# Performance work log

Measured on AMD Instinct MI355X. Metric: run time of the kernel, lower is better.

Reference implementation:

```python
import jax, jax.numpy as jnp
import numpy as np

HIDDEN = 512

def setup_inputs() -> dict:
    key = jax.random.key(0)
    ks = jax.random.split(key, 6)
    B, T = 65536, 100
    scale = 0.1  # keep tanh MLP in a sane dynamic range
    return {
        "y0": jax.random.normal(ks[0], (B, 2), jnp.float32),
        "t_points": jnp.arange(T, dtype=jnp.float32) * 0.01,
        "W1": jax.random.normal(ks[1], (2, HIDDEN), jnp.float32) * scale,
        "b1": jnp.zeros((HIDDEN,), jnp.float32),
        "W2": jax.random.normal(ks[2], (HIDDEN, HIDDEN), jnp.float32) * scale,
        "b2": jnp.zeros((HIDDEN,), jnp.float32),
        "W3": jax.random.normal(ks[3], (HIDDEN, HIDDEN // 2), jnp.float32) * scale,
        "b3": jnp.zeros((HIDDEN // 2,), jnp.float32),
        "W4": jax.random.normal(ks[4], (HIDDEN // 2, 2), jnp.float32) * scale,
        "b4": jnp.zeros((2,), jnp.float32),
    }

def _mlp(y, W1, b1, W2, b2, W3, b3, W4, b4):
    # 4-layer tanh MLP: 2 -> H -> H -> H//2 -> 2 (t is unused in ODEFunc)
    h = jnp.tanh(y @ W1 + b1)
    h = jnp.tanh(h @ W2 + b2)
    h = jnp.tanh(h @ W3 + b3)
    return h @ W4 + b4

def reference(y0, t_points, W1, b1, W2, b2, W3, b3, W4, b4):
    f = lambda y: _mlp(y, W1, b1, W2, b2, W3, b3, W4, b4)
    dts = t_points[1:] - t_points[:-1]  # [T-1]

    def step(y, dt):
        k1 = f(y)
        k2 = f(y + k1 * (dt * 0.5))
        k3 = f(y + k2 * (dt * 0.5))
        k4 = f(y + k3 * dt)
        y_next = y + (dt / 6.0) * (k1 + 2.0 * k2 + 2.0 * k3 + k4)
        return y_next, y_next

    _, traj = jax.lax.scan(step, y0, dts)
    return jnp.concatenate([y0[None], traj], axis=0)  # [T, B, 2]
```

## Files before the change

kernel.cpp:

```cpp
#include <hip/hip_runtime.h>
#include <hip/hip_bf16.h>
#include <stdint.h>

using bfrag_t = __attribute__((ext_vector_type(8))) short;
using f32x4   = __attribute__((ext_vector_type(4))) float;

#define HID  512
#define H3   256
#define RB   128
#define NTH  512
#define KSC  2.885390081777927f

static __device__ __forceinline__ uint32_t bf16_rne(float f) {
    uint32_t u = __float_as_uint(f);
    return (u + 0x7fffu + ((u >> 16) & 1u)) >> 16;
}
static __device__ __forceinline__ uint32_t pk_bf16(float a, float b) {
    union { __hip_bfloat162 h; uint32_t u; } c;
    c.h = __float22bfloat162_rn(make_float2(a, b));
    return c.u;
}
static __device__ __forceinline__ float fast_exp2(float x) {
#if __has_builtin(__builtin_amdgcn_exp2f)
    return __builtin_amdgcn_exp2f(x);
#else
    return exp2f(x);
#endif
}
static __device__ __forceinline__ float fast_rcp(float x) {
#if __has_builtin(__builtin_amdgcn_rcpf)
    return __builtin_amdgcn_rcpf(x);
#else
    return 1.0f / x;
#endif
}
static __device__ __forceinline__ float ftanh_s(float xs) {
    float e = fast_exp2(xs);
    return 1.0f - 2.0f * fast_rcp(e + 1.0f);
}
static __device__ __forceinline__ bfrag_t frag_of(uint4 v) {
    union { uint4 u; bfrag_t f; } c; c.u = v; return c.f;
}

__global__ void prep_weights(const float* __restrict__ W1, const float* __restrict__ b1,
                             const float* __restrict__ W2, const float* __restrict__ b2,
                             const float* __restrict__ W3, const float* __restrict__ b3,
                             uint4* __restrict__ o2, uint4* __restrict__ o3,
                             float* __restrict__ w1p, float* __restrict__ b2s,
                             float* __restrict__ b3s)
{
    int id = blockIdx.x * 256 + threadIdx.x;
    if (id < 32768) {
        int l = id & 63, kt = (id >> 6) & 15, mt = id >> 10;
        int m = mt * 16 + (l & 15), k0 = kt * 32 + (l >> 4) * 8;
        uint32_t p[4];
        #pragma unroll
        for (int jj = 0; jj < 4; ++jj) {
            float v0 = KSC * W2[(k0 + jj * 2    ) * 512 + m];
            float v1 = KSC * W2[(k0 + jj * 2 + 1) * 512 + m];
            p[jj] = bf16_rne(v0) | (bf16_rne(v1) << 16);
        }
        o2[id] = make_uint4(p[0], p[1], p[2], p[3]);
    } else if (id < 49152) {
        int id2 = id - 32768;
        int l = id2 & 63, kt = (id2 >> 6) & 15, mt = id2 >> 10;
        int m = mt * 16 + (l & 15), k0 = kt * 32 + (l >> 4) * 8;
        uint32_t p[4];
        #pragma unroll
        for (int jj = 0; jj < 4; ++jj) {
            float v0 = KSC * W3[(k0 + jj * 2    ) * 256 + m];
            float v1 = KSC * W3[(k0 + jj * 2 + 1) * 256 + m];
            p[jj] = bf16_rne(v0) | (bf16_rne(v1) << 16);
        }
        o3[id2] = make_uint4(p[0], p[1], p[2], p[3]);
    } else if (id < 49152 + 1536) {
        int t = id - 49152;
        int ck = t / 24, j = t % 24;
        int f = ck * 8 + (j & 7);
        float v = (j < 8) ? W1[f] : (j < 16) ? W1[512 + f] : b1[f];
        w1p[t] = KSC * v;
    } else if (id < 49152 + 1536 + 512) {
        int i = id - 49152 - 1536; b2s[i] = KSC * b2[i];
    } else if (id < 49152 + 1536 + 512 + 256) {
        int i = id - 49152 - 1536 - 512; b3s[i] = KSC * b3[i];
    }
}

struct SmemT {
    uint4  hbuf[64 * RB];
    float  b2[HID];
    float  b3[H3];
    float  y [RB][2];
    float  z [RB][2];
    float  ya[RB][2];
    float  part[4][RB][2];
};

__global__ __launch_bounds__(NTH, 2) void node_kernel(
    const float* __restrict__ y0, const float* __restrict__ tp,
    const float* __restrict__ W4g, const float* __restrict__ b4g,
    const uint4* __restrict__ w2A, const uint4* __restrict__ w3A,
    const float* __restrict__ w1p, const float* __restrict__ b2s,
    const float* __restrict__ b3s,
    float* __restrict__ out, int Bn, int T)
{
    __shared__ SmemT s;
    const int tid = threadIdx.x;
    const int l   = tid & 63;
    const int w   = tid >> 6;
    const int wu  = __builtin_amdgcn_readfirstlane(w);
    const int b0  = blockIdx.x * RB;

    for (int i = tid; i < HID; i += NTH) s.b2[i] = b2s[i];
    for (int i = tid; i < H3;  i += NTH) s.b3[i] = b3s[i];
    if (tid < RB) {
        float2 v = ((const float2*)y0)[b0 + tid];
        s.y[tid][0] = v.x; s.y[tid][1] = v.y;
        ((float2*)out)[b0 + tid] = v;
    }
    __syncthreads();

    const float* w1w = w1p + wu * 8 * 24;

    for (int st = 0; st < T - 1; ++st) {
        float dt = tp[st + 1] - tp[st];
        if (tid < RB) {
            s.z [tid][0] = s.y[tid][0]; s.z [tid][1] = s.y[tid][1];
            s.ya[tid][0] = s.y[tid][0]; s.ya[tid][1] = s.y[tid][1];
        }
        __syncthreads();

        for (int e = 0; e < 4; ++e) {
            {
                float zl0 = s.z[l][0],      zl1 = s.z[l][1];
                float zh0 = s.z[64 + l][0], zh1 = s.z[64 + l][1];
                #pragma unroll
                for (int i = 0; i < 8; ++i) {
                    const float* P = w1w + i * 24;
                    int ck = wu * 8 + i;
                    float xa[8], xb[8];
                    #pragma unroll
                    for (int jj = 0; jj < 8; ++jj) {
                        float wa = P[jj], wb = P[8 + jj], bb = P[16 + jj];
                        xa[jj] = ftanh_s(fmaf(zl0, wa, fmaf(zl1, wb, bb)));
                        xb[jj] = ftanh_s(fmaf(zh0, wa, fmaf(zh1, wb, bb)));
                    }
                    s.hbuf[ck * RB + l] = make_uint4(
                        pk_bf16(xa[0], xa[1]), pk_bf16(xa[2], xa[3]),
                        pk_bf16(xa[4], xa[5]), pk_bf16(xa[6], xa[7]));
                    s.hbuf[ck * RB + 64 + l] = make_uint4(
                        pk_bf16(xb[0], xb[1]), pk_bf16(xb[2], xb[3]),
                        pk_bf16(xb[4], xb[5]), pk_bf16(xb[6], xb[7]));
                }
            }
            __syncthreads();

            {
                const int q = l >> 4, rr = l & 15;
                f32x4 acc[4][8];
                #pragma unroll
                for (int mt = 0; mt < 4; ++mt) {
                    int mb = (w * 4 + mt) * 16 + q * 4;
                    float4 bi = *(const float4*)&s.b2[mb];
                    #pragma unroll
                    for (int nt = 0; nt < 8; ++nt) acc[mt][nt] = (f32x4){bi.x, bi.y, bi.z, bi.w};
                }
                uint4 aC[4], aN[4];
                #pragma unroll
                for (int mt = 0; mt < 4; ++mt) aC[mt] = w2A[((w * 4 + mt) * 16) * 64 + l];
                for (int kt = 0; kt < 16; ++kt) {
                    uint4 bF[8];
                    #pragma unroll
                    for (int nt = 0; nt < 8; ++nt)
                        bF[nt] = s.hbuf[(kt * 4 + q) * RB + nt * 16 + rr];
                    if (kt < 15) {
                        #pragma unroll
                        for (int mt = 0; mt < 4; ++mt)
                            aN[mt] = w2A[(((w * 4 + mt) * 16) + kt + 1) * 64 + l];
                    }
                    #pragma unroll
                    for (int mt = 0; mt < 4; ++mt)
                        #pragma unroll
                        for (int nt = 0; nt < 8; ++nt)
                            acc[mt][nt] = __builtin_amdgcn_mfma_f32_16x16x32_bf16(
                                frag_of(aC[mt]), frag_of(bF[nt]), acc[mt][nt], 0, 0, 0);
                    #pragma unroll
                    for (int mt = 0; mt < 4; ++mt) aC[mt] = aN[mt];
                }
                __syncthreads();
                #pragma unroll
                for (int mt = 0; mt < 4; ++mt) {
                    int mb = (w * 4 + mt) * 16 + q * 4;
                    int ck = mb >> 3, hi = (mb >> 2) & 1;
                    #pragma unroll
                    for (int nt = 0; nt < 8; ++nt) {
                        int n = nt * 16 + rr;
                        f32x4 c = acc[mt][nt];
                        uint32_t u0 = pk_bf16(ftanh_s(c[0]), ftanh_s(c[1]));
                        uint32_t u1 = pk_bf16(ftanh_s(c[2]), ftanh_s(c[3]));
                        ((uint2*)s.hbuf)[((ck * RB + n) << 1) | hi] = make_uint2(u0, u1);
                    }
                }
                __syncthreads();
            }

            {
                const int q = l >> 4, rr = l & 15;
                const int mg = w >> 1, ng = w & 1;
                f32x4 acc[4][4];
                #pragma unroll
                for (int mt = 0; mt < 4; ++mt) {
                    int mb = (mg * 4 + mt) * 16 + q * 4;
                    float4 bi = *(const float4*)&s.b3[mb];
                    #pragma unroll
                    for (int nt = 0; nt < 4; ++nt) acc[mt][nt] = (f32x4){bi.x, bi.y, bi.z, bi.w};
                }
                uint4 aC[4], aN[4];
                #pragma unroll
                for (int mt = 0; mt < 4; ++mt) aC[mt] = w3A[((mg * 4 + mt) * 16) * 64 + l];
                for (int kt = 0; kt < 16; ++kt) {
                    uint4 bF[4];
                    #pragma unroll
                    for (int nt = 0; nt < 4; ++nt)
                        bF[nt] = s.hbuf[(kt * 4 + q) * RB + ng * 64 + nt * 16 + rr];
                    if (kt < 15) {
                        #pragma unroll
                        for (int mt = 0; mt < 4; ++mt)
                            aN[mt] = w3A[(((mg * 4 + mt) * 16) + kt + 1) * 64 + l];
                    }
                    #pragma unroll
                    for (int mt = 0; mt < 4; ++mt)
                        #pragma unroll
                        for (int nt = 0; nt < 4; ++nt)
                            acc[mt][nt] = __builtin_amdgcn_mfma_f32_16x16x32_bf16(
                                frag_of(aC[mt]), frag_of(bF[nt]), acc[mt][nt], 0, 0, 0);
                    #pragma unroll
                    for (int mt = 0; mt < 4; ++mt) aC[mt] = aN[mt];
                }
                __syncthreads();
                #pragma unroll
                for (int mt = 0; mt < 4; ++mt) {
                    int mb = (mg * 4 + mt) * 16 + q * 4;
                    int ck = mb >> 3, hi = (mb >> 2) & 1;
                    #pragma unroll
                    for (int nt = 0; nt < 4; ++nt) {
                        int n = ng * 64 + nt * 16 + rr;
                        f32x4 c = acc[mt][nt];
                        uint32_t u0 = pk_bf16(ftanh_s(c[0]), ftanh_s(c[1]));
                        uint32_t u1 = pk_bf16(ftanh_s(c[2]), ftanh_s(c[3]));
                        ((uint2*)s.hbuf)[((ck * RB + n) << 1) | hi] = make_uint2(u0, u1);
                    }
                }
                __syncthreads();
            }

            {
                int r  = tid & 127;
                int qq = __builtin_amdgcn_readfirstlane(tid >> 7);
                float a0 = 0.f, a1 = 0.f;
                #pragma unroll
                for (int j = 0; j < 8; ++j) {
                    int ck = qq * 8 + j;
                    uint4 hv = s.hbuf[ck * RB + r];
                    const uint32_t* pu = (const uint32_t*)&hv;
                    #pragma unroll
                    for (int jj = 0; jj < 4; ++jj) {
                        uint32_t uu = pu[jj];
                        float h0 = __uint_as_float(uu << 16);
                        float h1 = __uint_as_float(uu & 0xffff0000u);
                        int f = ck * 8 + jj * 2;
                        a0 = fmaf(h0, W4g[f * 2],     fmaf(h1, W4g[f * 2 + 2], a0));
                        a1 = fmaf(h0, W4g[f * 2 + 1], fmaf(h1, W4g[f * 2 + 3], a1));
                    }
                }
                s.part[qq][r][0] = a0; s.part[qq][r][1] = a1;
            }
            __syncthreads();

            if (tid < RB) {
                float k0 = s.part[0][tid][0] + s.part[1][tid][0]
                         + s.part[2][tid][0] + s.part[3][tid][0] + b4g[0];
                float k1 = s.part[0][tid][1] + s.part[1][tid][1]
                         + s.part[2][tid][1] + s.part[3][tid][1] + b4g[1];
                float wg = (e == 0 || e == 3) ? dt * (1.f / 6.f) : dt * (1.f / 3.f);
                s.ya[tid][0] += wg * k0; s.ya[tid][1] += wg * k1;
                if (e < 3) {
                    float aa = (e == 2) ? dt : dt * 0.5f;
                    s.z[tid][0] = s.y[tid][0] + aa * k0;
                    s.z[tid][1] = s.y[tid][1] + aa * k1;
                } else {
                    s.y[tid][0] = s.ya[tid][0]; s.y[tid][1] = s.ya[tid][1];
                    ((float2*)out)[(size_t)(st + 1) * Bn + b0 + tid] =
                        make_float2(s.ya[tid][0], s.ya[tid][1]);
                }
            }
            __syncthreads();
        }
    }
}

extern "C" void kernel_launch(void* const* d_in, const int* in_sizes, int n_in,
                              void* d_out, int out_size, void* d_ws, size_t ws_size,
                              hipStream_t stream)
{
    const float* y0 = (const float*)d_in[0];
    const float* tp = (const float*)d_in[1];
    const float* W1 = (const float*)d_in[2];
    const float* b1 = (const float*)d_in[3];
    const float* W2 = (const float*)d_in[4];
    const float* b2 = (const float*)d_in[5];
    const float* W3 = (const float*)d_in[6];
    const float* b3 = (const float*)d_in[7];
    const float* W4 = (const float*)d_in[8];
    const float* b4 = (const float*)d_in[9];
    float* out = (float*)d_out;

    const int Bn = in_sizes[0] / 2;
    const int T  = in_sizes[1];

    uint4* w2A = (uint4*)d_ws;
    uint4* w3A = w2A + 32768;
    float* w1p = (float*)(w3A + 16384);
    float* b2s = w1p + 1536;
    float* b3s = b2s + 512;

    prep_weights<<<201, 256, 0, stream>>>(W1, b1, W2, b2, W3, b3,
                                          w2A, w3A, w1p, b2s, b3s);
    node_kernel<<<Bn / RB, NTH, 0, stream>>>(y0, tp, W4, b4,
                                             w2A, w3A, w1p, b2s, b3s, out, Bn, T);
}
```

Measured before the change: 26.28 ms.

## Split block rows into two half-batches and interleave MLP stages across them

Each block's 128 rows are split into two 64-row halves with separate hidden buffers, and the RK4 MLP evaluation is software-pipelined so one half's layer-3/layer-4 work overlaps the other half's layer-1/layer-2 work between barriers. The goal is to fill the serial phases (scalar tanh layer 1, the W4 reduction and the RK update), which otherwise leave MFMA units idle, with independent matrix work from the other half. The cost is narrower MFMA tiles per half (fewer B-fragment reuses per weight load, so w2A/w3A are reloaded twice as often), more shared memory, and a more complicated schedule.

```diff
diff --git a/kernel.cpp b/kernel.cpp
--- a/kernel.cpp
+++ b/kernel.cpp
@@ -7,7 +7,7 @@
 
 #define HID  512
 #define H3   256
-#define RB   128
+#define RB   64
 #define NTH  512
 #define KSC  2.885390081777927f
 
@@ -87,14 +87,206 @@
 }
 
 struct SmemT {
-    uint4  hbuf[64 * RB];
+    uint4  hA[64 * RB];
+    uint4  hB[64 * RB];
     float  b2[HID];
     float  b3[H3];
-    float  y [RB][2];
-    float  z [RB][2];
-    float  ya[RB][2];
-    float  part[4][RB][2];
+    float  y [128][2];
+    float  z [128][2];
+    float  ya[128][2];
+    float  part[8][RB][2];
 };
+
+static __device__ __forceinline__ void s1_stage(uint4* __restrict__ h,
+                                                const float* __restrict__ zrow,
+                                                const float* __restrict__ w1w,
+                                                int l, int wu)
+{
+    float z0 = zrow[2 * l], z1 = zrow[2 * l + 1];
+    #pragma unroll
+    for (int i = 0; i < 8; ++i) {
+        const float* P = w1w + i * 24;
+        int ck = wu * 8 + i;
+        float x[8];
+        #pragma unroll
+        for (int jj = 0; jj < 8; ++jj)
+            x[jj] = ftanh_s(fmaf(z0, P[jj], fmaf(z1, P[8 + jj], P[16 + jj])));
+        h[ck * RB + l] = make_uint4(pk_bf16(x[0], x[1]), pk_bf16(x[2], x[3]),
+                                    pk_bf16(x[4], x[5]), pk_bf16(x[6], x[7]));
+    }
+}
+
+static __device__ __forceinline__ void s2_mfma(const uint4* __restrict__ h,
+                                               const uint4* __restrict__ w2A,
+                                               const float* __restrict__ b2,
+                                               f32x4 (&acc)[4][4],
+                                               int l, int w, int q, int rr)
+{
+    #pragma unroll
+    for (int mt = 0; mt < 4; ++mt) {
+        int mb = (w * 4 + mt) * 16 + q * 4;
+        float4 bi = *(const float4*)&b2[mb];
+        #pragma unroll
+        for (int nt = 0; nt < 4; ++nt) acc[mt][nt] = (f32x4){bi.x, bi.y, bi.z, bi.w};
+    }
+    uint4 aC[4], aN[4];
+    #pragma unroll
+    for (int mt = 0; mt < 4; ++mt) aC[mt] = w2A[((w * 4 + mt) * 16) * 64 + l];
+    for (int kt = 0; kt < 16; ++kt) {
+        uint4 bF[4];
+        #pragma unroll
+        for (int nt = 0; nt < 4; ++nt)
+            bF[nt] = h[(kt * 4 + q) * RB + nt * 16 + rr];
+        if (kt < 15) {
+            #pragma unroll
+            for (int mt = 0; mt < 4; ++mt)
+                aN[mt] = w2A[(((w * 4 + mt) * 16) + kt + 1) * 64 + l];
+        }
+        #pragma unroll
+        for (int mt = 0; mt < 4; ++mt)
+            #pragma unroll
+            for (int nt = 0; nt < 4; ++nt)
+                acc[mt][nt] = __builtin_amdgcn_mfma_f32_16x16x32_bf16(
+                    frag_of(aC[mt]), frag_of(bF[nt]), acc[mt][nt], 0, 0, 0);
+        #pragma unroll
+        for (int mt = 0; mt < 4; ++mt) aC[mt] = aN[mt];
+    }
+}
+
+static __device__ __forceinline__ void s2_epi(uint4* __restrict__ h,
+                                              f32x4 (&acc)[4][4],
+                                              int w, int q, int rr)
+{
+    #pragma unroll
+    for (int mt = 0; mt < 4; ++mt) {
+        int mb = (w * 4 + mt) * 16 + q * 4;
+        int ck = mb >> 3, hi = (mb >> 2) & 1;
+        #pragma unroll
+        for (int nt = 0; nt < 4; ++nt) {
+            int n = nt * 16 + rr;
+            f32x4 c = acc[mt][nt];
+            uint32_t u0 = pk_bf16(ftanh_s(c[0]), ftanh_s(c[1]));
+            uint32_t u1 = pk_bf16(ftanh_s(c[2]), ftanh_s(c[3]));
+            ((uint2*)h)[((ck * RB + n) << 1) | hi] = make_uint2(u0, u1);
+        }
+    }
+}
+
+static __device__ __forceinline__ void s3_mfma(const uint4* __restrict__ h,
+                                               const uint4* __restrict__ w3A,
+                                               const float* __restrict__ b3,
+                                               f32x4 (&acc)[2][4],
+                                               int l, int w, int q, int rr)
+{
+    #pragma unroll
+    for (int mt = 0; mt < 2; ++mt) {
+        int mb = (w * 2 + mt) * 16 + q * 4;
+        float4 bi = *(const float4*)&b3[mb];
+        #pragma unroll
+        for (int nt = 0; nt < 4; ++nt) acc[mt][nt] = (f32x4){bi.x, bi.y, bi.z, bi.w};
+    }
+    uint4 aC[2], aN[2];
+    #pragma unroll
+    for (int mt = 0; mt < 2; ++mt) aC[mt] = w3A[((w * 2 + mt) * 16) * 64 + l];
+    for (int kt = 0; kt < 16; ++kt) {
+        uint4 bF[4];
+        #pragma unroll
+        for (int nt = 0; nt < 4; ++nt)
+            bF[nt] = h[(kt * 4 + q) * RB + nt * 16 + rr];
+        if (kt < 15) {
+            #pragma unroll
+            for (int mt = 0; mt < 2; ++mt)
+                aN[mt] = w3A[(((w * 2 + mt) * 16) + kt + 1) * 64 + l];
+        }
+        #pragma unroll
+        for (int mt = 0; mt < 2; ++mt)
+            #pragma unroll
+            for (int nt = 0; nt < 4; ++nt)
+                acc[mt][nt] = __builtin_amdgcn_mfma_f32_16x16x32_bf16(
+                    frag_of(aC[mt]), frag_of(bF[nt]), acc[mt][nt], 0, 0, 0);
+        #pragma unroll
+        for (int mt = 0; mt < 2; ++mt) aC[mt] = aN[mt];
+    }
+}
+
+static __device__ __forceinline__ void s3_epi(uint4* __restrict__ h,
+                                              f32x4 (&acc)[2][4],
+                                              int w, int q, int rr)
+{
+    #pragma unroll
+    for (int mt = 0; mt < 2; ++mt) {
+        int mb = (w * 2 + mt) * 16 + q * 4;
+        int ck = mb >> 3, hi = (mb >> 2) & 1;
+        #pragma unroll
+        for (int nt = 0; nt < 4; ++nt) {
+            int n = nt * 16 + rr;
+            f32x4 c = acc[mt][nt];
+            uint32_t u0 = pk_bf16(ftanh_s(c[0]), ftanh_s(c[1]));
+            uint32_t u1 = pk_bf16(ftanh_s(c[2]), ftanh_s(c[3]));
+            ((uint2*)h)[((ck * RB + n) << 1) | hi] = make_uint2(u0, u1);
+        }
+    }
+}
+
+static __device__ __forceinline__ void s4_part(const uint4* __restrict__ h,
+                                               float* __restrict__ part,
+                                               const float* __restrict__ W4g,
+                                               int tid)
+{
+    int r  = tid & 63;
+    int qq = __builtin_amdgcn_readfirstlane(tid >> 6);
+    float a0 = 0.f, a1 = 0.f;
+    #pragma unroll
+    for (int j = 0; j < 4; ++j) {
+        int ck = qq * 4 + j;
+        uint4 hv = h[ck * RB + r];
+        const uint32_t* pu = (const uint32_t*)&hv;
+        #pragma unroll
+        for (int jj = 0; jj < 4; ++jj) {
+            uint32_t uu = pu[jj];
+            float h0 = __uint_as_float(uu << 16);
+            float h1 = __uint_as_float(uu & 0xffff0000u);
+            int f = ck * 8 + jj * 2;
+            a0 = fmaf(h0, W4g[f * 2],     fmaf(h1, W4g[f * 2 + 2], a0));
+            a1 = fmaf(h0, W4g[f * 2 + 1], fmaf(h1, W4g[f * 2 + 3], a1));
+        }
+    }
+    part[(qq * RB + r) * 2    ] = a0;
+    part[(qq * RB + r) * 2 + 1] = a1;
+}
+
+static __device__ __forceinline__ void s4_fin(float* __restrict__ yS, float* __restrict__ zS,
+                                              float* __restrict__ yaS,
+                                              const float* __restrict__ part,
+                                              const float* __restrict__ tp,
+                                              const float* __restrict__ b4g,
+                                              float* __restrict__ out,
+                                              int g, int Bn, int rowg, int tid)
+{
+    if (tid < RB) {
+        int r = tid;
+        float k0 = b4g[0], k1 = b4g[1];
+        #pragma unroll
+        for (int qq = 0; qq < 8; ++qq) {
+            k0 += part[(qq * RB + r) * 2];
+            k1 += part[(qq * RB + r) * 2 + 1];
+        }
+        int st = g >> 2, e = g & 3;
+        float dt = tp[st + 1] - tp[st];
+        float wg = (e == 0 || e == 3) ? dt * (1.f / 6.f) : dt * (1.f / 3.f);
+        float ya0 = yaS[2 * r] + wg * k0, ya1 = yaS[2 * r + 1] + wg * k1;
+        yaS[2 * r] = ya0; yaS[2 * r + 1] = ya1;
+        if (e < 3) {
+            float aa = (e == 2) ? dt : dt * 0.5f;
+            zS[2 * r] = yS[2 * r] + aa * k0;
+            zS[2 * r + 1] = yS[2 * r + 1] + aa * k1;
+        } else {
+            yS[2 * r] = ya0; yS[2 * r + 1] = ya1;
+            zS[2 * r] = ya0; zS[2 * r + 1] = ya1;
+            ((float2*)out)[(size_t)(st + 1) * Bn + rowg + r] = make_float2(ya0, ya1);
+        }
+    }
+}
 
 __global__ __launch_bounds__(NTH, 2) void node_kernel(
     const float* __restrict__ y0, const float* __restrict__ tp,
@@ -109,191 +301,65 @@
     const int l   = tid & 63;
     const int w   = tid >> 6;
     const int wu  = __builtin_amdgcn_readfirstlane(w);
-    const int b0  = blockIdx.x * RB;
+    const int q   = l >> 4, rr = l & 15;
+    const int b0  = blockIdx.x * 128;
 
     for (int i = tid; i < HID; i += NTH) s.b2[i] = b2s[i];
     for (int i = tid; i < H3;  i += NTH) s.b3[i] = b3s[i];
-    if (tid < RB) {
+    if (tid < 128) {
         float2 v = ((const float2*)y0)[b0 + tid];
         s.y[tid][0] = v.x; s.y[tid][1] = v.y;
+        s.z[tid][0] = v.x; s.z[tid][1] = v.y;
+        s.ya[tid][0] = v.x; s.ya[tid][1] = v.y;
         ((float2*)out)[b0 + tid] = v;
     }
     __syncthreads();
 
-    const float* w1w = w1p + wu * 8 * 24;
-
-    for (int st = 0; st < T - 1; ++st) {
-        float dt = tp[st + 1] - tp[st];
-        if (tid < RB) {
-            s.z [tid][0] = s.y[tid][0]; s.z [tid][1] = s.y[tid][1];
-            s.ya[tid][0] = s.y[tid][0]; s.ya[tid][1] = s.y[tid][1];
-        }
-        __syncthreads();
-
-        for (int e = 0; e < 4; ++e) {
-            {
-                float zl0 = s.z[l][0],      zl1 = s.z[l][1];
-                float zh0 = s.z[64 + l][0], zh1 = s.z[64 + l][1];
-                #pragma unroll
-                for (int i = 0; i < 8; ++i) {
-                    const float* P = w1w + i * 24;
-                    int ck = wu * 8 + i;
-                    float xa[8], xb[8];
-                    #pragma unroll
-                    for (int jj = 0; jj < 8; ++jj) {
-                        float wa = P[jj], wb = P[8 + jj], bb = P[16 + jj];
-                        xa[jj] = ftanh_s(fmaf(zl0, wa, fmaf(zl1, wb, bb)));
-                        xb[jj] = ftanh_s(fmaf(zh0, wa, fmaf(zh1, wb, bb)));
-                    }
-                    s.hbuf[ck * RB + l] = make_uint4(
-                        pk_bf16(xa[0], xa[1]), pk_bf16(xa[2], xa[3]),
-                        pk_bf16(xa[4], xa[5]), pk_bf16(xa[6], xa[7]));
-                    s.hbuf[ck * RB + 64 + l] = make_uint4(
-                        pk_bf16(xb[0], xb[1]), pk_bf16(xb[2], xb[3]),
-                        pk_bf16(xb[4], xb[5]), pk_bf16(xb[6], xb[7]));
-                }
-            }
-            __syncthreads();
-
-            {
-                const int q = l >> 4, rr = l & 15;
-                f32x4 acc[4][8];
-                #pragma unroll
-                for (int mt = 0; mt < 4; ++mt) {
-                    int mb = (w * 4 + mt) * 16 + q * 4;
-                    float4 bi = *(const float4*)&s.b2[mb];
-                    #pragma unroll
-                    for (int nt = 0; nt < 8; ++nt) acc[mt][nt] = (f32x4){bi.x, bi.y, bi.z, bi.w};
-                }
-                uint4 aC[4], aN[4];
-                #pragma unroll
-                for (int mt = 0; mt < 4; ++mt) aC[mt] = w2A[((w * 4 + mt) * 16) * 64 + l];
-                for (int kt = 0; kt < 16; ++kt) {
-                    uint4 bF[8];
-                    #pragma unroll
-                    for (int nt = 0; nt < 8; ++nt)
-                        bF[nt] = s.hbuf[(kt * 4 + q) * RB + nt * 16 + rr];
-                    if (kt < 15) {
-                        #pragma unroll
-                        for (int mt = 0; mt < 4; ++mt)
-                            aN[mt] = w2A[(((w * 4 + mt) * 16) + kt + 1) * 64 + l];
-                    }
-                    #pragma unroll
-                    for (int mt = 0; mt < 4; ++mt)
-                        #pragma unroll
-                        for (int nt = 0; nt < 8; ++nt)
-                            acc[mt][nt] = __builtin_amdgcn_mfma_f32_16x16x32_bf16(
-                                frag_of(aC[mt]), frag_of(bF[nt]), acc[mt][nt], 0, 0, 0);
-                    #pragma unroll
-                    for (int mt = 0; mt < 4; ++mt) aC[mt] = aN[mt];
-                }
-                __syncthreads();
-                #pragma unroll
-                for (int mt = 0; mt < 4; ++mt) {
-                    int mb = (w * 4 + mt) * 16 + q * 4;
-                    int ck = mb >> 3, hi = (mb >> 2) & 1;
-                    #pragma unroll
-                    for (int nt = 0; nt < 8; ++nt) {
-                        int n = nt * 16 + rr;
-                        f32x4 c = acc[mt][nt];
-                        uint32_t u0 = pk_bf16(ftanh_s(c[0]), ftanh_s(c[1]));
-                        uint32_t u1 = pk_bf16(ftanh_s(c[2]), ftanh_s(c[3]));
-                        ((uint2*)s.hbuf)[((ck * RB + n) << 1) | hi] = make_uint2(u0, u1);
-                    }
-                }
-                __syncthreads();
-            }
-
-            {
-                const int q = l >> 4, rr = l & 15;
-                const int mg = w >> 1, ng = w & 1;
-                f32x4 acc[4][4];
-                #pragma unroll
-                for (int mt = 0; mt < 4; ++mt) {
-                    int mb = (mg * 4 + mt) * 16 + q * 4;
-                    float4 bi = *(const float4*)&s.b3[mb];
-                    #pragma unroll
-                    for (int nt = 0; nt < 4; ++nt) acc[mt][nt] = (f32x4){bi.x, bi.y, bi.z, bi.w};
-                }
-                uint4 aC[4], aN[4];
-                #pragma unroll
-                for (int mt = 0; mt < 4; ++mt) aC[mt] = w3A[((mg * 4 + mt) * 16) * 64 + l];
-                for (int kt = 0; kt < 16; ++kt) {
-                    uint4 bF[4];
-                    #pragma unroll
-                    for (int nt = 0; nt < 4; ++nt)
-                        bF[nt] = s.hbuf[(kt * 4 + q) * RB + ng * 64 + nt * 16 + rr];
-                    if (kt < 15) {
-                        #pragma unroll
-                        for (int mt = 0; mt < 4; ++mt)
-                            aN[mt] = w3A[(((mg * 4 + mt) * 16) + kt + 1) * 64 + l];
-                    }
-                    #pragma unroll
-                    for (int mt = 0; mt < 4; ++mt)
-                        #pragma unroll
-                        for (int nt = 0; nt < 4; ++nt)
-                            acc[mt][nt] = __builtin_amdgcn_mfma_f32_16x16x32_bf16(
-                                frag_of(aC[mt]), frag_of(bF[nt]), acc[mt][nt], 0, 0, 0);
-                    #pragma unroll
-                    for (int mt = 0; mt < 4; ++mt) aC[mt] = aN[mt];
-                }
-                __syncthreads();
-                #pragma unroll
-                for (int mt = 0; mt < 4; ++mt) {
-                    int mb = (mg * 4 + mt) * 16 + q * 4;
-                    int ck = mb >> 3, hi = (mb >> 2) & 1;
-                    #pragma unroll
-                    for (int nt = 0; nt < 4; ++nt) {
-                        int n = ng * 64 + nt * 16 + rr;
-                        f32x4 c = acc[mt][nt];
-                        uint32_t u0 = pk_bf16(ftanh_s(c[0]), ftanh_s(c[1]));
-                        uint32_t u1 = pk_bf16(ftanh_s(c[2]), ftanh_s(c[3]));
-                        ((uint2*)s.hbuf)[((ck * RB + n) << 1) | hi] = make_uint2(u0, u1);
-                    }
-                }
-                __syncthreads();
-            }
-
-            {
-                int r  = tid & 127;
-                int qq = __builtin_amdgcn_readfirstlane(tid >> 7);
-                float a0 = 0.f, a1 = 0.f;
-                #pragma unroll
-                for (int j = 0; j < 8; ++j) {
-                    int ck = qq * 8 + j;
-                    uint4 hv = s.hbuf[ck * RB + r];
-                    const uint32_t* pu = (const uint32_t*)&hv;
-                    #pragma unroll
-                    for (int jj = 0; jj < 4; ++jj) {
-                        uint32_t uu = pu[jj];
-                        float h0 = __uint_as_float(uu << 16);
-                        float h1 = __uint_as_float(uu & 0xffff0000u);
-                        int f = ck * 8 + jj * 2;
-                        a0 = fmaf(h0, W4g[f * 2],     fmaf(h1, W4g[f * 2 + 2], a0));
-                        a1 = fmaf(h0, W4g[f * 2 + 1], fmaf(h1, W4g[f * 2 + 3], a1));
-                    }
-                }
-                s.part[qq][r][0] = a0; s.part[qq][r][1] = a1;
-            }
-            __syncthreads();
-
-            if (tid < RB) {
-                float k0 = s.part[0][tid][0] + s.part[1][tid][0]
-                         + s.part[2][tid][0] + s.part[3][tid][0] + b4g[0];
-                float k1 = s.part[0][tid][1] + s.part[1][tid][1]
-                         + s.part[2][tid][1] + s.part[3][tid][1] + b4g[1];
-                float wg = (e == 0 || e == 3) ? dt * (1.f / 6.f) : dt * (1.f / 3.f);
-                s.ya[tid][0] += wg * k0; s.ya[tid][1] += wg * k1;
-                if (e < 3) {
-                    float aa = (e == 2) ? dt : dt * 0.5f;
-                    s.z[tid][0] = s.y[tid][0] + aa * k0;
-                    s.z[tid][1] = s.y[tid][1] + aa * k1;
-                } else {
-                    s.y[tid][0] = s.ya[tid][0]; s.y[tid][1] = s.ya[tid][1];
-                    ((float2*)out)[(size_t)(st + 1) * Bn + b0 + tid] =
-                        make_float2(s.ya[tid][0], s.ya[tid][1]);
-                }
-            }
+    const float* w1w = w1p + wu * 192;
+    float* part = &s.part[0][0][0];
+    const int E = (T - 1) * 4;
+
+    for (int ea = 0; ea <= E; ++ea) {
+        const bool doA = (ea < E), doB = (ea > 0);
+        const int gB = ea - 1;
+
+        {
+            f32x4 c3[2][4];
+            if (doB) s3_mfma(s.hB, w3A, s.b3, c3, l, w, q, rr);
+            if (doA) s1_stage(s.hA, &s.z[0][0], w1w, l, wu);
+            __syncthreads();
+            if (doB) s3_epi(s.hB, c3, w, q, rr);
+            __syncthreads();
+        }
+
+        {
+            f32x4 c2[4][4];
+            if (doA) s2_mfma(s.hA, w2A, s.b2, c2, l, w, q, rr);
+            if (doB) s4_part(s.hB, part, W4g, tid);
+            __syncthreads();
+            if (doA) s2_epi(s.hA, c2, w, q, rr);
+            if (doB) s4_fin(&s.y[64][0], &s.z[64][0], &s.ya[64][0], part,
+                            tp, b4g, out, gB, Bn, b0 + 64, tid);
+            __syncthreads();
+        }
+
+        {
+            f32x4 c3[2][4];
+            if (doA) s3_mfma(s.hA, w3A, s.b3, c3, l, w, q, rr);
+            if (doA) s1_stage(s.hB, &s.z[64][0], w1w, l, wu);
+            __syncthreads();
+            if (doA) s3_epi(s.hA, c3, w, q, rr);
+            __syncthreads();
+        }
+
+        {
+            f32x4 c2[4][4];
+            if (doA) s2_mfma(s.hB, w2A, s.b2, c2, l, w, q, rr);
+            if (doA) s4_part(s.hA, part, W4g, tid);
+            __syncthreads();
+            if (doA) s2_epi(s.hB, c2, w, q, rr);
+            if (doA) s4_fin(&s.y[0][0], &s.z[0][0], &s.ya[0][0], part,
+                            tp, b4g, out, ea, Bn, b0, tid);
             __syncthreads();
         }
     }
@@ -326,6 +392,6 @@
 
     prep_weights<<<201, 256, 0, stream>>>(W1, b1, W2, b2, W3, b3,
                                           w2A, w3A, w1p, b2s, b3s);
-    node_kernel<<<Bn / RB, NTH, 0, stream>>>(y0, tp, W4, b4,
-                                             w2A, w3A, w1p, b2s, b3s, out, Bn, T);
-}
+    node_kernel<<<Bn / 128, NTH, 0, stream>>>(y0, tp, W4, b4,
+                                              w2A, w3A, w1p, b2s, b3s, out, Bn, T);
+}
```

Measured after the change: 67.70 ms. 158% more time.

## Halve rows per block and switch layer GEMMs to 32x32x16 MFMA tiles

Applied to the files above, without the earlier changes.

Block row count drops from 128 to 64, and the hidden-layer GEMMs now use 32x32x16 bf16 MFMA with 16-wide accumulators instead of 16x16x32 tiles. The weight pre-pack layout is rewritten to match, and launch bounds now ask for 4 blocks per CU. The intent is more resident blocks per CU to hide latency and fewer, larger MFMA ops. In exchange, each weight fragment read from global memory is reused across half as many rows, so weight traffic per row doubles. The W4 reduction is split over 8 waves and reads its weights as float4.

```diff
diff --git a/kernel.cpp b/kernel.cpp
--- a/kernel.cpp
+++ b/kernel.cpp
@@ -3,11 +3,11 @@
 #include <stdint.h>
 
 using bfrag_t = __attribute__((ext_vector_type(8))) short;
-using f32x4   = __attribute__((ext_vector_type(4))) float;
+using f32x16  = __attribute__((ext_vector_type(16))) float;
 
 #define HID  512
 #define H3   256
-#define RB   128
+#define RB   64
 #define NTH  512
 #define KSC  2.885390081777927f
 
@@ -51,8 +51,8 @@
 {
     int id = blockIdx.x * 256 + threadIdx.x;
     if (id < 32768) {
-        int l = id & 63, kt = (id >> 6) & 15, mt = id >> 10;
-        int m = mt * 16 + (l & 15), k0 = kt * 32 + (l >> 4) * 8;
+        int l = id & 63, kt = (id >> 6) & 31, mt = id >> 11;
+        int m = mt * 32 + (l & 31), k0 = kt * 16 + (l >> 5) * 8;
         uint32_t p[4];
         #pragma unroll
         for (int jj = 0; jj < 4; ++jj) {
@@ -63,8 +63,8 @@
         o2[id] = make_uint4(p[0], p[1], p[2], p[3]);
     } else if (id < 49152) {
         int id2 = id - 32768;
-        int l = id2 & 63, kt = (id2 >> 6) & 15, mt = id2 >> 10;
-        int m = mt * 16 + (l & 15), k0 = kt * 32 + (l >> 4) * 8;
+        int l = id2 & 63, kt = (id2 >> 6) & 31, mt = id2 >> 11;
+        int m = mt * 32 + (l & 31), k0 = kt * 16 + (l >> 5) * 8;
         uint32_t p[4];
         #pragma unroll
         for (int jj = 0; jj < 4; ++jj) {
@@ -93,10 +93,10 @@
     float  y [RB][2];
     float  z [RB][2];
     float  ya[RB][2];
-    float  part[4][RB][2];
+    float  part[8][RB][2];
 };
 
-__global__ __launch_bounds__(NTH, 2) void node_kernel(
+__global__ __launch_bounds__(NTH, 4) void node_kernel(
     const float* __restrict__ y0, const float* __restrict__ tp,
     const float* __restrict__ W4g, const float* __restrict__ b4g,
     const uint4* __restrict__ w2A, const uint4* __restrict__ w3A,
@@ -109,6 +109,7 @@
     const int l   = tid & 63;
     const int w   = tid >> 6;
     const int wu  = __builtin_amdgcn_readfirstlane(w);
+    const int q2  = l >> 5, r32 = l & 31;
     const int b0  = blockIdx.x * RB;
 
     for (int i = tid; i < HID; i += NTH) s.b2[i] = b2s[i];
@@ -120,7 +121,7 @@
     }
     __syncthreads();
 
-    const float* w1w = w1p + wu * 8 * 24;
+    const float* w1w = w1p + wu * 192;
 
     for (int st = 0; st < T - 1; ++st) {
         float dt = tp[st + 1] - tp[st];
@@ -132,135 +133,134 @@
 
         for (int e = 0; e < 4; ++e) {
             {
-                float zl0 = s.z[l][0],      zl1 = s.z[l][1];
-                float zh0 = s.z[64 + l][0], zh1 = s.z[64 + l][1];
+                float z0 = s.z[l][0], z1 = s.z[l][1];
                 #pragma unroll
                 for (int i = 0; i < 8; ++i) {
                     const float* P = w1w + i * 24;
                     int ck = wu * 8 + i;
-                    float xa[8], xb[8];
-                    #pragma unroll
-                    for (int jj = 0; jj < 8; ++jj) {
-                        float wa = P[jj], wb = P[8 + jj], bb = P[16 + jj];
-                        xa[jj] = ftanh_s(fmaf(zl0, wa, fmaf(zl1, wb, bb)));
-                        xb[jj] = ftanh_s(fmaf(zh0, wa, fmaf(zh1, wb, bb)));
-                    }
+                    float x[8];
+                    #pragma unroll
+                    for (int jj = 0; jj < 8; ++jj)
+                        x[jj] = ftanh_s(fmaf(z0, P[jj], fmaf(z1, P[8 + jj], P[16 + jj])));
                     s.hbuf[ck * RB + l] = make_uint4(
-                        pk_bf16(xa[0], xa[1]), pk_bf16(xa[2], xa[3]),
-                        pk_bf16(xa[4], xa[5]), pk_bf16(xa[6], xa[7]));
-                    s.hbuf[ck * RB + 64 + l] = make_uint4(
-                        pk_bf16(xb[0], xb[1]), pk_bf16(xb[2], xb[3]),
-                        pk_bf16(xb[4], xb[5]), pk_bf16(xb[6], xb[7]));
+                        pk_bf16(x[0], x[1]), pk_bf16(x[2], x[3]),
+                        pk_bf16(x[4], x[5]), pk_bf16(x[6], x[7]));
                 }
             }
             __syncthreads();
 
             {
-                const int q = l >> 4, rr = l & 15;
-                f32x4 acc[4][8];
-                #pragma unroll
-                for (int mt = 0; mt < 4; ++mt) {
-                    int mb = (w * 4 + mt) * 16 + q * 4;
-                    float4 bi = *(const float4*)&s.b2[mb];
-                    #pragma unroll
-                    for (int nt = 0; nt < 8; ++nt) acc[mt][nt] = (f32x4){bi.x, bi.y, bi.z, bi.w};
-                }
-                uint4 aC[4], aN[4];
-                #pragma unroll
-                for (int mt = 0; mt < 4; ++mt) aC[mt] = w2A[((w * 4 + mt) * 16) * 64 + l];
-                for (int kt = 0; kt < 16; ++kt) {
-                    uint4 bF[8];
-                    #pragma unroll
-                    for (int nt = 0; nt < 8; ++nt)
-                        bF[nt] = s.hbuf[(kt * 4 + q) * RB + nt * 16 + rr];
-                    if (kt < 15) {
+                f32x16 acc[2][2];
+                #pragma unroll
+                for (int mt = 0; mt < 2; ++mt) {
+                    int mbase = (wu * 2 + mt) * 32;
+                    #pragma unroll
+                    for (int r2 = 0; r2 < 4; ++r2) {
+                        float4 bi = *(const float4*)&s.b2[mbase + 8 * r2 + 4 * q2];
                         #pragma unroll
-                        for (int mt = 0; mt < 4; ++mt)
-                            aN[mt] = w2A[(((w * 4 + mt) * 16) + kt + 1) * 64 + l];
-                    }
-                    #pragma unroll
-                    for (int mt = 0; mt < 4; ++mt)
+                        for (int nt = 0; nt < 2; ++nt) {
+                            acc[mt][nt][4 * r2 + 0] = bi.x;
+                            acc[mt][nt][4 * r2 + 1] = bi.y;
+                            acc[mt][nt][4 * r2 + 2] = bi.z;
+                            acc[mt][nt][4 * r2 + 3] = bi.w;
+                        }
+                    }
+                }
+                uint4 aC[2], aN[2];
+                aC[0] = w2A[((wu * 2 + 0) * 32) * 64 + l];
+                aC[1] = w2A[((wu * 2 + 1) * 32) * 64 + l];
+                for (int kt = 0; kt < 32; ++kt) {
+                    uint4 bF0 = s.hbuf[(kt * 2 + q2) * RB + r32];
+                    uint4 bF1 = s.hbuf[(kt * 2 + q2) * RB + 32 + r32];
+                    if (kt < 31) {
+                        aN[0] = w2A[((wu * 2 + 0) * 32 + kt + 1) * 64 + l];
+                        aN[1] = w2A[((wu * 2 + 1) * 32 + kt + 1) * 64 + l];
+                    }
+                    acc[0][0] = __builtin_amdgcn_mfma_f32_32x32x16_bf16(
+                        frag_of(aC[0]), frag_of(bF0), acc[0][0], 0, 0, 0);
+                    acc[0][1] = __builtin_amdgcn_mfma_f32_32x32x16_bf16(
+                        frag_of(aC[0]), frag_of(bF1), acc[0][1], 0, 0, 0);
+                    acc[1][0] = __builtin_amdgcn_mfma_f32_32x32x16_bf16(
+                        frag_of(aC[1]), frag_of(bF0), acc[1][0], 0, 0, 0);
+                    acc[1][1] = __builtin_amdgcn_mfma_f32_32x32x16_bf16(
+                        frag_of(aC[1]), frag_of(bF1), acc[1][1], 0, 0, 0);
+                    aC[0] = aN[0]; aC[1] = aN[1];
+                }
+                __syncthreads();
+                #pragma unroll
+                for (int mt = 0; mt < 2; ++mt) {
+                    int cb = (wu * 2 + mt) * 4;
+                    #pragma unroll
+                    for (int nt = 0; nt < 2; ++nt) {
+                        int n = nt * 32 + r32;
                         #pragma unroll
-                        for (int nt = 0; nt < 8; ++nt)
-                            acc[mt][nt] = __builtin_amdgcn_mfma_f32_16x16x32_bf16(
-                                frag_of(aC[mt]), frag_of(bF[nt]), acc[mt][nt], 0, 0, 0);
-                    #pragma unroll
-                    for (int mt = 0; mt < 4; ++mt) aC[mt] = aN[mt];
+                        for (int r2 = 0; r2 < 4; ++r2) {
+                            float t0 = ftanh_s(acc[mt][nt][4 * r2 + 0]);
+                            float t1 = ftanh_s(acc[mt][nt][4 * r2 + 1]);
+                            float t2 = ftanh_s(acc[mt][nt][4 * r2 + 2]);
+                            float t3 = ftanh_s(acc[mt][nt][4 * r2 + 3]);
+                            ((uint2*)s.hbuf)[(((cb + r2) * RB + n) << 1) | q2] =
+                                make_uint2(pk_bf16(t0, t1), pk_bf16(t2, t3));
+                        }
+                    }
                 }
                 __syncthreads();
-                #pragma unroll
-                for (int mt = 0; mt < 4; ++mt) {
-                    int mb = (w * 4 + mt) * 16 + q * 4;
-                    int ck = mb >> 3, hi = (mb >> 2) & 1;
-                    #pragma unroll
-                    for (int nt = 0; nt < 8; ++nt) {
-                        int n = nt * 16 + rr;
-                        f32x4 c = acc[mt][nt];
-                        uint32_t u0 = pk_bf16(ftanh_s(c[0]), ftanh_s(c[1]));
-                        uint32_t u1 = pk_bf16(ftanh_s(c[2]), ftanh_s(c[3]));
-                        ((uint2*)s.hbuf)[((ck * RB + n) << 1) | hi] = make_uint2(u0, u1);
-                    }
+            }
+
+            {
+                f32x16 acc[2];
+                {
+                    int mbase = wu * 32;
+                    #pragma unroll
+                    for (int r2 = 0; r2 < 4; ++r2) {
+                        float4 bi = *(const float4*)&s.b3[mbase + 8 * r2 + 4 * q2];
+                        #pragma unroll
+                        for (int nt = 0; nt < 2; ++nt) {
+                            acc[nt][4 * r2 + 0] = bi.x;
+                            acc[nt][4 * r2 + 1] = bi.y;
+                            acc[nt][4 * r2 + 2] = bi.z;
+                            acc[nt][4 * r2 + 3] = bi.w;
+                        }
+                    }
+                }
+                uint4 aC = w3A[(wu * 32) * 64 + l], aN;
+                for (int kt = 0; kt < 32; ++kt) {
+                    uint4 bF0 = s.hbuf[(kt * 2 + q2) * RB + r32];
+                    uint4 bF1 = s.hbuf[(kt * 2 + q2) * RB + 32 + r32];
+                    if (kt < 31) aN = w3A[(wu * 32 + kt + 1) * 64 + l];
+                    acc[0] = __builtin_amdgcn_mfma_f32_32x32x16_bf16(
+                        frag_of(aC), frag_of(bF0), acc[0], 0, 0, 0);
+                    acc[1] = __builtin_amdgcn_mfma_f32_32x32x16_bf16(
+                        frag_of(aC), frag_of(bF1), acc[1], 0, 0, 0);
+                    aC = aN;
                 }
                 __syncthreads();
+                {
+                    int cb = wu * 4;
+                    #pragma unroll
+                    for (int nt = 0; nt < 2; ++nt) {
+                        int n = nt * 32 + r32;
+                        #pragma unroll
+                        for (int r2 = 0; r2 < 4; ++r2) {
+                            float t0 = ftanh_s(acc[nt][4 * r2 + 0]);
+                            float t1 = ftanh_s(acc[nt][4 * r2 + 1]);
+                            float t2 = ftanh_s(acc[nt][4 * r2 + 2]);
+                            float t3 = ftanh_s(acc[nt][4 * r2 + 3]);
+                            ((uint2*)s.hbuf)[(((cb + r2) * RB + n) << 1) | q2] =
+                                make_uint2(pk_bf16(t0, t1), pk_bf16(t2, t3));
+                        }
+                    }
+                }
+                __syncthreads();
             }
 
             {
-                const int q = l >> 4, rr = l & 15;
-                const int mg = w >> 1, ng = w & 1;
-                f32x4 acc[4][4];
-                #pragma unroll
-                for (int mt = 0; mt < 4; ++mt) {
-                    int mb = (mg * 4 + mt) * 16 + q * 4;
-                    float4 bi = *(const float4*)&s.b3[mb];
-                    #pragma unroll
-                    for (int nt = 0; nt < 4; ++nt) acc[mt][nt] = (f32x4){bi.x, bi.y, bi.z, bi.w};
-                }
-                uint4 aC[4], aN[4];
-                #pragma unroll
-                for (int mt = 0; mt < 4; ++mt) aC[mt] = w3A[((mg * 4 + mt) * 16) * 64 + l];
-                for (int kt = 0; kt < 16; ++kt) {
-                    uint4 bF[4];
-                    #pragma unroll
-                    for (int nt = 0; nt < 4; ++nt)
-                        bF[nt] = s.hbuf[(kt * 4 + q) * RB + ng * 64 + nt * 16 + rr];
-                    if (kt < 15) {
-                        #pragma unroll
-                        for (int mt = 0; mt < 4; ++mt)
-                            aN[mt] = w3A[(((mg * 4 + mt) * 16) + kt + 1) * 64 + l];
-                    }
-                    #pragma unroll
-                    for (int mt = 0; mt < 4; ++mt)
-                        #pragma unroll
-                        for (int nt = 0; nt < 4; ++nt)
-                            acc[mt][nt] = __builtin_amdgcn_mfma_f32_16x16x32_bf16(
-                                frag_of(aC[mt]), frag_of(bF[nt]), acc[mt][nt], 0, 0, 0);
-                    #pragma unroll
-                    for (int mt = 0; mt < 4; ++mt) aC[mt] = aN[mt];
-                }
-                __syncthreads();
-                #pragma unroll
-                for (int mt = 0; mt < 4; ++mt) {
-                    int mb = (mg * 4 + mt) * 16 + q * 4;
-                    int ck = mb >> 3, hi = (mb >> 2) & 1;
-                    #pragma unroll
-                    for (int nt = 0; nt < 4; ++nt) {
-                        int n = ng * 64 + nt * 16 + rr;
-                        f32x4 c = acc[mt][nt];
-                        uint32_t u0 = pk_bf16(ftanh_s(c[0]), ftanh_s(c[1]));
-                        uint32_t u1 = pk_bf16(ftanh_s(c[2]), ftanh_s(c[3]));
-                        ((uint2*)s.hbuf)[((ck * RB + n) << 1) | hi] = make_uint2(u0, u1);
-                    }
-                }
-                __syncthreads();
-            }
-
-            {
-                int r  = tid & 127;
-                int qq = __builtin_amdgcn_readfirstlane(tid >> 7);
+                int r  = tid & 63;
+                int qq = __builtin_amdgcn_readfirstlane(tid >> 6);
                 float a0 = 0.f, a1 = 0.f;
                 #pragma unroll
-                for (int j = 0; j < 8; ++j) {
-                    int ck = qq * 8 + j;
+                for (int j = 0; j < 4; ++j) {
+                    int ck = qq * 4 + j;
                     uint4 hv = s.hbuf[ck * RB + r];
                     const uint32_t* pu = (const uint32_t*)&hv;
                     #pragma unroll
@@ -269,8 +269,9 @@
                         float h0 = __uint_as_float(uu << 16);
                         float h1 = __uint_as_float(uu & 0xffff0000u);
                         int f = ck * 8 + jj * 2;
-                        a0 = fmaf(h0, W4g[f * 2],     fmaf(h1, W4g[f * 2 + 2], a0));
-                        a1 = fmaf(h0, W4g[f * 2 + 1], fmaf(h1, W4g[f * 2 + 3], a1));
+                        float4 w4 = *(const float4*)&W4g[f * 2];
+                        a0 = fmaf(h0, w4.x, fmaf(h1, w4.z, a0));
+                        a1 = fmaf(h0, w4.y, fmaf(h1, w4.w, a1));
                     }
                 }
                 s.part[qq][r][0] = a0; s.part[qq][r][1] = a1;
@@ -278,10 +279,12 @@
             __syncthreads();
 
             if (tid < RB) {
-                float k0 = s.part[0][tid][0] + s.part[1][tid][0]
-                         + s.part[2][tid][0] + s.part[3][tid][0] + b4g[0];
-                float k1 = s.part[0][tid][1] + s.part[1][tid][1]
-                         + s.part[2][tid][1] + s.part[3][tid][1] + b4g[1];
+                float k0 = b4g[0], k1 = b4g[1];
+                #pragma unroll
+                for (int qq = 0; qq < 8; ++qq) {
+                    k0 += s.part[qq][tid][0];
+                    k1 += s.part[qq][tid][1];
+                }
                 float wg = (e == 0 || e == 3) ? dt * (1.f / 6.f) : dt * (1.f / 3.f);
                 s.ya[tid][0] += wg * k0; s.ya[tid][1] += wg * k1;
                 if (e < 3) {
```

New measurement: 30.02 ms. 1.14x slower.
